# Kernel tuning notes

Measured on AMD Instinct MI355X. Metric: run time of the kernel, lower is better.

Reference implementation:

```python
import jax, jax.numpy as jnp
import numpy as np

B, T, C, H = 2, 2048, 1024, 16
D = C // H  # head_dim = 64


def setup_inputs() -> dict:
    key = jax.random.key(0)
    ks = jax.random.split(key, 5)
    x = jax.random.normal(ks[0], (B, T, C), dtype=jnp.float32)
    # fused QKV projection: Linear(C, 3C)
    W_qkv = jax.random.normal(ks[1], (C, 3 * C), dtype=jnp.float32) / np.sqrt(C)
    b_qkv = jax.random.normal(ks[2], (3 * C,), dtype=jnp.float32) * 0.02
    # output projection: Linear(C, C)
    W_proj = jax.random.normal(ks[3], (C, C), dtype=jnp.float32) / np.sqrt(C)
    b_proj = jax.random.normal(ks[4], (C,), dtype=jnp.float32) * 0.02
    return {"x": x, "W_qkv": W_qkv, "b_qkv": b_qkv, "W_proj": W_proj, "b_proj": b_proj}


def reference(x, W_qkv, b_qkv, W_proj, b_proj):
    # fused QKV projection
    qkv = jnp.einsum("btc,cd->btd", x, W_qkv) + b_qkv  # [B,T,3C]
    q, k, v = jnp.split(qkv, 3, axis=-1)
    # [B,T,C] -> [B,H,T,D]
    def to_heads(t):
        return t.reshape(B, T, H, D).transpose(0, 2, 1, 3)
    q, k, v = to_heads(q), to_heads(k), to_heads(v)
    # causal scaled dot-product attention (SDPA default scale = 1/sqrt(head_dim))
    scale = 1.0 / np.sqrt(D).astype(np.float32)
    scores = jnp.einsum("bhqd,bhkd->bhqk", q, k) * scale  # [B,H,T,T]
    causal = jnp.tril(jnp.ones((T, T), dtype=bool))
    scores = jnp.where(causal, scores, jnp.finfo(scores.dtype).min)
    attn = jax.nn.softmax(scores, axis=-1)
    out = jnp.einsum("bhqk,bhkd->bhqd", attn, v)  # [B,H,T,D]
    out = out.transpose(0, 2, 1, 3).reshape(B, T, C)
    # output projection
    return jnp.einsum("btc,cd->btd", out, W_proj) + b_proj
```

## Files before the change

kernel.cpp:

```cpp
#include <hip/hip_runtime.h>
#include <hip/hip_bf16.h>

typedef __attribute__((ext_vector_type(8))) __bf16 bf16x8;
typedef __attribute__((ext_vector_type(8))) short short8;
typedef __attribute__((ext_vector_type(4))) float f32x4;
typedef __attribute__((ext_vector_type(4))) short sh4;

typedef __attribute__((address_space(1))) void GVoid;
typedef __attribute__((address_space(3))) void LVoid;

#define NEGBIG (-1e30f)
#define SCL 0.18033688011112042f

constexpr int TT = 2048, CC = 1024, HH = 16, DD = 64, C3 = 3072;

__device__ __forceinline__ unsigned short f2bf(float f) {
  unsigned int i = __float_as_uint(f);
  return (unsigned short)((i + 0x7FFFu + ((i >> 16) & 1u)) >> 16);
}
__device__ __forceinline__ unsigned short f2bf_tr(float f) {
  return (unsigned short)(__float_as_uint(f) >> 16);
}
__device__ __forceinline__ void async16(const void* g, void* l) {
  __builtin_amdgcn_global_load_lds((GVoid*)g, (LVoid*)l, 16, 0, 0);
}

__global__ __launch_bounds__(256) void cvt_bf16(
    const float* __restrict__ in, unsigned short* __restrict__ out, int n8)
{
  const int i = blockIdx.x * 256 + threadIdx.x;
  if (i >= n8) return;
  const float* p = in + (size_t)i * 8;
  f32x4 a = *(const f32x4*)p, b = *(const f32x4*)(p + 4);
  sh4 r0, r1;
  ((unsigned short*)&r0)[0] = f2bf(a[0]); ((unsigned short*)&r0)[1] = f2bf(a[1]);
  ((unsigned short*)&r0)[2] = f2bf(a[2]); ((unsigned short*)&r0)[3] = f2bf(a[3]);
  ((unsigned short*)&r1)[0] = f2bf(b[0]); ((unsigned short*)&r1)[1] = f2bf(b[1]);
  ((unsigned short*)&r1)[2] = f2bf(b[2]); ((unsigned short*)&r1)[3] = f2bf(b[3]);
  *(sh4*)(out + (size_t)i * 8) = r0;
  *(sh4*)(out + (size_t)i * 8 + 4) = r1;
}

__global__ __launch_bounds__(256) void transpose_cvt(
    const float* __restrict__ in, unsigned short* __restrict__ out, int R, int Cd)
{
  __shared__ __align__(16) unsigned short tile[64 * 72];
  const int r0 = blockIdx.y * 64, c0 = blockIdx.x * 64;
  const int tid = threadIdx.x;
#pragma unroll
  for (int r = 0; r < 2; ++r) {
    const int elem = r * 2048 + tid * 8;
    const int ii = elem >> 6, jj = elem & 63;
    const float* p = in + (size_t)(r0 + ii) * Cd + c0 + jj;
    f32x4 a = *(const f32x4*)p, b = *(const f32x4*)(p + 4);
    short8 v;
    ((unsigned short*)&v)[0] = f2bf(a[0]); ((unsigned short*)&v)[1] = f2bf(a[1]);
    ((unsigned short*)&v)[2] = f2bf(a[2]); ((unsigned short*)&v)[3] = f2bf(a[3]);
    ((unsigned short*)&v)[4] = f2bf(b[0]); ((unsigned short*)&v)[5] = f2bf(b[1]);
    ((unsigned short*)&v)[6] = f2bf(b[2]); ((unsigned short*)&v)[7] = f2bf(b[3]);
    *(short8*)&tile[ii * 72 + jj] = v;
  }
  __syncthreads();
#pragma unroll
  for (int r = 0; r < 2; ++r) {
    const int elem = r * 2048 + tid * 8;
    const int jj = elem >> 6, ii0 = elem & 63;
    short8 v;
#pragma unroll
    for (int e = 0; e < 8; ++e) ((unsigned short*)&v)[e] = tile[(ii0 + e) * 72 + jj];
    *(short8*)&out[(size_t)(c0 + jj) * R + r0 + ii0] = v;
  }
}

template <int MODE>
__global__ __launch_bounds__(256) void gemm_bt(
    const unsigned short* __restrict__ A,
    const unsigned short* __restrict__ Bt,
    const float* __restrict__ bias,
    void* __restrict__ Cp, unsigned short* __restrict__ Vt,
    int M, int N, int K, int lda)
{
  __shared__ __align__(16) unsigned short sA[128 * 32];
  __shared__ __align__(16) unsigned short sB[128 * 32];
  const int tid = threadIdx.x;
  const int w = tid >> 6, l = tid & 63, ln = l & 15, quad = l >> 4;
  const int wm = w >> 1, wn = w & 1;
  const int m0 = blockIdx.y * 128, n0 = blockIdx.x * 128;
  f32x4 acc[4][4] = {};

  for (int k0 = 0; k0 < K; k0 += 32) {
    __syncthreads();
#pragma unroll
    for (int r = 0; r < 2; ++r) {
      const int elem = r * 2048 + tid * 8;
      const int ar = elem >> 5, ac = elem & 31;
      async16(A  + (size_t)(m0 + ar) * lda + k0 + ac, sA + r * 2048 + w * 512);
      async16(Bt + (size_t)(n0 + ar) * K   + k0 + ac, sB + r * 2048 + w * 512);
    }
    __syncthreads();

    bf16x8 af[4], bfr[4];
#pragma unroll
    for (int i = 0; i < 4; i++)
      af[i] = *(const bf16x8*)&sA[(wm * 64 + i * 16 + ln) * 32 + quad * 8];
#pragma unroll
    for (int j = 0; j < 4; j++)
      bfr[j] = *(const bf16x8*)&sB[(wn * 64 + j * 16 + ln) * 32 + quad * 8];
#pragma unroll
    for (int i = 0; i < 4; i++)
#pragma unroll
      for (int j = 0; j < 4; j++)
        acc[i][j] = __builtin_amdgcn_mfma_f32_16x16x32_bf16(af[i], bfr[j], acc[i][j], 0, 0, 0);
  }

  float bj[4];
#pragma unroll
  for (int j = 0; j < 4; j++) bj[j] = bias[n0 + wn * 64 + j * 16 + ln];

#pragma unroll
  for (int i = 0; i < 4; i++)
#pragma unroll
    for (int g = 0; g < 4; ++g) {
      const int gm = m0 + wm * 64 + i * 16 + quad * 4 + g;
#pragma unroll
      for (int j = 0; j < 4; j++) {
        const int gn = n0 + wn * 64 + j * 16 + ln;
        float v = acc[i][j][g] + bj[j];
        if (MODE == 0) {
          if (gn < 2048) {
            if (gn < 1024) v *= SCL;
            ((unsigned short*)Cp)[(size_t)gm * 2048 + gn] = f2bf(v);
          } else {
            const int hh = (gn >> 6) & 15, dd = gn & 63;
            const int bb = gm >> 11, t = gm & 2047;
            Vt[((size_t)((bb * HH + hh) * DD + dd)) * TT + t] = f2bf(v);
          }
        } else {
          ((float*)Cp)[(size_t)gm * N + gn] = v;
        }
      }
    }
}

__global__ __launch_bounds__(512) void attn128(
    unsigned short* __restrict__ QK, const unsigned short* __restrict__ Vt)
{
  __shared__ __align__(16) unsigned short kt[2][64 * 72];
  __shared__ __align__(16) unsigned short vt[2][80 * 72];
  __shared__ __align__(16) unsigned short pt[8][16 * 72];
  const int pair = blockIdx.x, bh = blockIdx.y;
  const int b = bh >> 4, h = bh & 15;
  const int tid = threadIdx.x, w = tid >> 6, l = tid & 63, ln = l & 15, quad = l >> 4;
  unsigned short*       Qp = QK + (size_t)b * TT * 2048 + h * DD;
  const unsigned short* Kp = QK + (size_t)b * TT * 2048 + CC + h * DD;
  const unsigned short* Vh = Vt + (size_t)bh * DD * TT;
  const int si = tid >> 3, so = (tid & 7) * 8;

  for (int idx = tid; idx < 16 * 72; idx += 512) {
    const unsigned short v = (idx < 72) ? (unsigned short)0x3F80 : (unsigned short)0;
    vt[0][64 * 72 + idx] = v;
    vt[1][64 * 72 + idx] = v;
  }

  for (int ph = 0; ph < 2; ++ph) {
    const int qt = ph ? 15 - pair : pair;
    const int qrow = qt * 128 + w * 16 + ln;
    bf16x8 qf0 = *(const bf16x8*)&Qp[(size_t)qrow * 2048 + quad * 8];
    bf16x8 qf1 = *(const bf16x8*)&Qp[(size_t)qrow * 2048 + 32 + quad * 8];

    f32x4 oacc[4] = {};
    f32x4 lacc = {};
    const int qg = qt * 128 + w * 16 + quad * 4;
    const int wfirst = qt * 128 + w * 16, wlast = wfirst + 15;
    const int kbmax = 2 * qt + 1;

    *(short8*)&kt[0][si * 72 + so] = *(const short8*)&Kp[(size_t)si * 2048 + so];
    *(short8*)&vt[0][si * 72 + so] = *(const short8*)&Vh[(size_t)si * TT + so];
    __syncthreads();

    for (int kb = 0; kb <= kbmax; ++kb) {
      const int cur = kb & 1;
      short8 pk, pv;
      if (kb < kbmax) {
        pk = *(const short8*)&Kp[(size_t)((kb + 1) * 64 + si) * 2048 + so];
        pv = *(const short8*)&Vh[(size_t)si * TT + (kb + 1) * 64 + so];
      }
      if (kb * 64 <= wlast) {
        f32x4 sacc[4] = {};
#pragma unroll
        for (int n = 0; n < 4; n++) {
          bf16x8 bk0 = *(const bf16x8*)&kt[cur][(n * 16 + ln) * 72 + quad * 8];
          bf16x8 bk1 = *(const bf16x8*)&kt[cur][(n * 16 + ln) * 72 + 32 + quad * 8];
          sacc[n] = __builtin_amdgcn_mfma_f32_16x16x32_bf16(qf0, bk0, sacc[n], 0, 0, 0);
          sacc[n] = __builtin_amdgcn_mfma_f32_16x16x32_bf16(qf1, bk1, sacc[n], 0, 0, 0);
        }
        if (kb * 64 + 63 > wfirst) {
#pragma unroll
          for (int n = 0; n < 4; n++) {
            const int keyg = kb * 64 + n * 16 + ln;
#pragma unroll
            for (int g = 0; g < 4; ++g)
              if (keyg > qg + g) sacc[n][g] = NEGBIG;
          }
        }
#pragma unroll
        for (int n = 0; n < 4; n++)
#pragma unroll
          for (int g = 0; g < 4; ++g)
            pt[w][(quad * 4 + g) * 72 + n * 16 + ln] = f2bf_tr(exp2f(sacc[n][g]));
        __builtin_amdgcn_wave_barrier();
        bf16x8 pf0 = *(const bf16x8*)&pt[w][ln * 72 + quad * 8];
        bf16x8 pf1 = *(const bf16x8*)&pt[w][ln * 72 + 32 + quad * 8];
#pragma unroll
        for (int n = 0; n < 4; n++) {
          bf16x8 bv0 = *(const bf16x8*)&vt[cur][(n * 16 + ln) * 72 + quad * 8];
          bf16x8 bv1 = *(const bf16x8*)&vt[cur][(n * 16 + ln) * 72 + 32 + quad * 8];
          oacc[n] = __builtin_amdgcn_mfma_f32_16x16x32_bf16(pf0, bv0, oacc[n], 0, 0, 0);
          oacc[n] = __builtin_amdgcn_mfma_f32_16x16x32_bf16(pf1, bv1, oacc[n], 0, 0, 0);
        }
        bf16x8 bl0 = *(const bf16x8*)&vt[cur][(64 + ln) * 72 + quad * 8];
        bf16x8 bl1 = *(const bf16x8*)&vt[cur][(64 + ln) * 72 + 32 + quad * 8];
        lacc = __builtin_amdgcn_mfma_f32_16x16x32_bf16(pf0, bl0, lacc, 0, 0, 0);
        lacc = __builtin_amdgcn_mfma_f32_16x16x32_bf16(pf1, bl1, lacc, 0, 0, 0);
      }
      if (kb < kbmax) {
        *(short8*)&kt[1 - cur][si * 72 + so] = pk;
        *(short8*)&vt[1 - cur][si * 72 + so] = pv;
      }
      __syncthreads();
    }
#pragma unroll
    for (int g = 0; g < 4; ++g) {
      const float lv = __shfl(lacc[g], l & 48);
      const float inv = 1.0f / lv;
      const int t = qg + g;
#pragma unroll
      for (int n = 0; n < 4; n++)
        Qp[(size_t)t * 2048 + n * 16 + ln] = f2bf(oacc[n][g] * inv);
    }
  }
}

extern "C" void kernel_launch(void* const* d_in, const int* in_sizes, int n_in,
                              void* d_out, int out_size, void* d_ws, size_t ws_size,
                              hipStream_t stream)
{
  (void)in_sizes; (void)n_in; (void)out_size; (void)ws_size;
  const float* x     = (const float*)d_in[0];
  const float* Wqkv  = (const float*)d_in[1];
  const float* bqkv  = (const float*)d_in[2];
  const float* Wproj = (const float*)d_in[3];
  const float* bproj = (const float*)d_in[4];

  unsigned short* QK     = (unsigned short*)d_ws;
  unsigned short* WqkvT  = QK + (size_t)4096 * 2048;
  unsigned short* WprojT = WqkvT;
  unsigned short* Vt = (unsigned short*)d_out;
  unsigned short* xb = Vt + (size_t)32 * 64 * 2048;

  cvt_bf16<<<dim3(4096 * 1024 / 8 / 256), 256, 0, stream>>>(x, xb, 4096 * 1024 / 8);
  transpose_cvt<<<dim3(C3 / 64, CC / 64), 256, 0, stream>>>(Wqkv, WqkvT, CC, C3);
  gemm_bt<0><<<dim3(C3 / 128, 4096 / 128), 256, 0, stream>>>(
      xb, WqkvT, bqkv, QK, Vt, 4096, C3, CC, CC);
  transpose_cvt<<<dim3(CC / 64, CC / 64), 256, 0, stream>>>(Wproj, WprojT, CC, CC);
  attn128<<<dim3(8, 2 * HH), 512, 0, stream>>>(QK, Vt);
  gemm_bt<1><<<dim3(CC / 128, 4096 / 128), 256, 0, stream>>>(
      QK, WprojT, bproj, d_out, nullptr, 4096, CC, CC, 2048);
}
```

Measured before the change: 208.7 us.

## Split attention into 64-row query tiles with heaviest-first block order

The attention kernel moves from 512-thread blocks that each process two paired 128-row query tiles to 256-thread blocks that each process one 64-row tile. Tiles are launched in reverse order so the longest causal tiles start first, and the grid grows from 256 to 1024 blocks. The aim is more blocks to spread across CUs and finer load balancing than the old pairing gave. In exchange, each K/V block staged in shared memory is reused by fewer query rows, so total K/V traffic roughly doubles.

```diff
diff --git a/kernel.cpp b/kernel.cpp
--- a/kernel.cpp
+++ b/kernel.cpp
@@ -142,102 +142,111 @@
     }
 }
 
-__global__ __launch_bounds__(512) void attn128(
+__global__ __launch_bounds__(256) void attn64(
     unsigned short* __restrict__ QK, const unsigned short* __restrict__ Vt)
 {
   __shared__ __align__(16) unsigned short kt[2][64 * 72];
   __shared__ __align__(16) unsigned short vt[2][80 * 72];
-  __shared__ __align__(16) unsigned short pt[8][16 * 72];
-  const int pair = blockIdx.x, bh = blockIdx.y;
+  __shared__ __align__(16) unsigned short pt[4][16 * 72];
+  const int tile = 31 - blockIdx.x;
+  const int bh = blockIdx.y;
   const int b = bh >> 4, h = bh & 15;
   const int tid = threadIdx.x, w = tid >> 6, l = tid & 63, ln = l & 15, quad = l >> 4;
   unsigned short*       Qp = QK + (size_t)b * TT * 2048 + h * DD;
   const unsigned short* Kp = QK + (size_t)b * TT * 2048 + CC + h * DD;
   const unsigned short* Vh = Vt + (size_t)bh * DD * TT;
-  const int si = tid >> 3, so = (tid & 7) * 8;
-
-  for (int idx = tid; idx < 16 * 72; idx += 512) {
+  const int si0 = tid >> 3, so = (tid & 7) * 8;
+
+  for (int idx = tid; idx < 16 * 72; idx += 256) {
     const unsigned short v = (idx < 72) ? (unsigned short)0x3F80 : (unsigned short)0;
     vt[0][64 * 72 + idx] = v;
     vt[1][64 * 72 + idx] = v;
   }
 
-  for (int ph = 0; ph < 2; ++ph) {
-    const int qt = ph ? 15 - pair : pair;
-    const int qrow = qt * 128 + w * 16 + ln;
-    bf16x8 qf0 = *(const bf16x8*)&Qp[(size_t)qrow * 2048 + quad * 8];
-    bf16x8 qf1 = *(const bf16x8*)&Qp[(size_t)qrow * 2048 + 32 + quad * 8];
-
-    f32x4 oacc[4] = {};
-    f32x4 lacc = {};
-    const int qg = qt * 128 + w * 16 + quad * 4;
-    const int wfirst = qt * 128 + w * 16, wlast = wfirst + 15;
-    const int kbmax = 2 * qt + 1;
-
+  const int qrow = tile * 64 + w * 16 + ln;
+  bf16x8 qf0 = *(const bf16x8*)&Qp[(size_t)qrow * 2048 + quad * 8];
+  bf16x8 qf1 = *(const bf16x8*)&Qp[(size_t)qrow * 2048 + 32 + quad * 8];
+
+  f32x4 oacc[4] = {};
+  f32x4 lacc = {};
+  const int qg = tile * 64 + w * 16 + quad * 4;
+  const int kbmax = tile;
+
+#pragma unroll
+  for (int r = 0; r < 2; ++r) {
+    const int si = si0 + 32 * r;
     *(short8*)&kt[0][si * 72 + so] = *(const short8*)&Kp[(size_t)si * 2048 + so];
     *(short8*)&vt[0][si * 72 + so] = *(const short8*)&Vh[(size_t)si * TT + so];
+  }
+  __syncthreads();
+
+  for (int kb = 0; kb <= kbmax; ++kb) {
+    const int cur = kb & 1;
+    short8 pk[2], pv[2];
+    if (kb < kbmax) {
+#pragma unroll
+      for (int r = 0; r < 2; ++r) {
+        const int si = si0 + 32 * r;
+        pk[r] = *(const short8*)&Kp[(size_t)((kb + 1) * 64 + si) * 2048 + so];
+        pv[r] = *(const short8*)&Vh[(size_t)si * TT + (kb + 1) * 64 + so];
+      }
+    }
+    {
+      f32x4 sacc[4] = {};
+#pragma unroll
+      for (int n = 0; n < 4; n++) {
+        bf16x8 bk0 = *(const bf16x8*)&kt[cur][(n * 16 + ln) * 72 + quad * 8];
+        bf16x8 bk1 = *(const bf16x8*)&kt[cur][(n * 16 + ln) * 72 + 32 + quad * 8];
+        sacc[n] = __builtin_amdgcn_mfma_f32_16x16x32_bf16(qf0, bk0, sacc[n], 0, 0, 0);
+        sacc[n] = __builtin_amdgcn_mfma_f32_16x16x32_bf16(qf1, bk1, sacc[n], 0, 0, 0);
+      }
+      if (kb == kbmax) {
+#pragma unroll
+        for (int n = 0; n < 4; n++) {
+          const int keyg = kb * 64 + n * 16 + ln;
+#pragma unroll
+          for (int g = 0; g < 4; ++g)
+            if (keyg > qg + g) sacc[n][g] = NEGBIG;
+        }
+      }
+#pragma unroll
+      for (int n = 0; n < 4; n++)
+#pragma unroll
+        for (int g = 0; g < 4; ++g)
+          pt[w][(quad * 4 + g) * 72 + n * 16 + ln] = f2bf_tr(exp2f(sacc[n][g]));
+      __builtin_amdgcn_wave_barrier();
+      bf16x8 pf0 = *(const bf16x8*)&pt[w][ln * 72 + quad * 8];
+      bf16x8 pf1 = *(const bf16x8*)&pt[w][ln * 72 + 32 + quad * 8];
+#pragma unroll
+      for (int n = 0; n < 4; n++) {
+        bf16x8 bv0 = *(const bf16x8*)&vt[cur][(n * 16 + ln) * 72 + quad * 8];
+        bf16x8 bv1 = *(const bf16x8*)&vt[cur][(n * 16 + ln) * 72 + 32 + quad * 8];
+        oacc[n] = __builtin_amdgcn_mfma_f32_16x16x32_bf16(pf0, bv0, oacc[n], 0, 0, 0);
+        oacc[n] = __builtin_amdgcn_mfma_f32_16x16x32_bf16(pf1, bv1, oacc[n], 0, 0, 0);
+      }
+      bf16x8 bl0 = *(const bf16x8*)&vt[cur][(64 + ln) * 72 + quad * 8];
+      bf16x8 bl1 = *(const bf16x8*)&vt[cur][(64 + ln) * 72 + 32 + quad * 8];
+      lacc = __builtin_amdgcn_mfma_f32_16x16x32_bf16(pf0, bl0, lacc, 0, 0, 0);
+      lacc = __builtin_amdgcn_mfma_f32_16x16x32_bf16(pf1, bl1, lacc, 0, 0, 0);
+    }
+    if (kb < kbmax) {
+#pragma unroll
+      for (int r = 0; r < 2; ++r) {
+        const int si = si0 + 32 * r;
+        *(short8*)&kt[1 - cur][si * 72 + so] = pk[r];
+        *(short8*)&vt[1 - cur][si * 72 + so] = pv[r];
+      }
+    }
     __syncthreads();
-
-    for (int kb = 0; kb <= kbmax; ++kb) {
-      const int cur = kb & 1;
-      short8 pk, pv;
-      if (kb < kbmax) {
-        pk = *(const short8*)&Kp[(size_t)((kb + 1) * 64 + si) * 2048 + so];
-        pv = *(const short8*)&Vh[(size_t)si * TT + (kb + 1) * 64 + so];
-      }
-      if (kb * 64 <= wlast) {
-        f32x4 sacc[4] = {};
-#pragma unroll
-        for (int n = 0; n < 4; n++) {
-          bf16x8 bk0 = *(const bf16x8*)&kt[cur][(n * 16 + ln) * 72 + quad * 8];
-          bf16x8 bk1 = *(const bf16x8*)&kt[cur][(n * 16 + ln) * 72 + 32 + quad * 8];
-          sacc[n] = __builtin_amdgcn_mfma_f32_16x16x32_bf16(qf0, bk0, sacc[n], 0, 0, 0);
-          sacc[n] = __builtin_amdgcn_mfma_f32_16x16x32_bf16(qf1, bk1, sacc[n], 0, 0, 0);
-        }
-        if (kb * 64 + 63 > wfirst) {
-#pragma unroll
-          for (int n = 0; n < 4; n++) {
-            const int keyg = kb * 64 + n * 16 + ln;
-#pragma unroll
-            for (int g = 0; g < 4; ++g)
-              if (keyg > qg + g) sacc[n][g] = NEGBIG;
-          }
-        }
-#pragma unroll
-        for (int n = 0; n < 4; n++)
-#pragma unroll
-          for (int g = 0; g < 4; ++g)
-            pt[w][(quad * 4 + g) * 72 + n * 16 + ln] = f2bf_tr(exp2f(sacc[n][g]));
-        __builtin_amdgcn_wave_barrier();
-        bf16x8 pf0 = *(const bf16x8*)&pt[w][ln * 72 + quad * 8];
-        bf16x8 pf1 = *(const bf16x8*)&pt[w][ln * 72 + 32 + quad * 8];
-#pragma unroll
-        for (int n = 0; n < 4; n++) {
-          bf16x8 bv0 = *(const bf16x8*)&vt[cur][(n * 16 + ln) * 72 + quad * 8];
-          bf16x8 bv1 = *(const bf16x8*)&vt[cur][(n * 16 + ln) * 72 + 32 + quad * 8];
-          oacc[n] = __builtin_amdgcn_mfma_f32_16x16x32_bf16(pf0, bv0, oacc[n], 0, 0, 0);
-          oacc[n] = __builtin_amdgcn_mfma_f32_16x16x32_bf16(pf1, bv1, oacc[n], 0, 0, 0);
-        }
-        bf16x8 bl0 = *(const bf16x8*)&vt[cur][(64 + ln) * 72 + quad * 8];
-        bf16x8 bl1 = *(const bf16x8*)&vt[cur][(64 + ln) * 72 + 32 + quad * 8];
-        lacc = __builtin_amdgcn_mfma_f32_16x16x32_bf16(pf0, bl0, lacc, 0, 0, 0);
-        lacc = __builtin_amdgcn_mfma_f32_16x16x32_bf16(pf1, bl1, lacc, 0, 0, 0);
-      }
-      if (kb < kbmax) {
-        *(short8*)&kt[1 - cur][si * 72 + so] = pk;
-        *(short8*)&vt[1 - cur][si * 72 + so] = pv;
-      }
-      __syncthreads();
-    }
-#pragma unroll
-    for (int g = 0; g < 4; ++g) {
-      const float lv = __shfl(lacc[g], l & 48);
-      const float inv = 1.0f / lv;
-      const int t = qg + g;
-#pragma unroll
-      for (int n = 0; n < 4; n++)
-        Qp[(size_t)t * 2048 + n * 16 + ln] = f2bf(oacc[n][g] * inv);
-    }
+  }
+#pragma unroll
+  for (int g = 0; g < 4; ++g) {
+    const float lv = __shfl(lacc[g], l & 48);
+    const float inv = 1.0f / lv;
+    const int t = qg + g;
+#pragma unroll
+    for (int n = 0; n < 4; n++)
+      Qp[(size_t)t * 2048 + n * 16 + ln] = f2bf(oacc[n][g] * inv);
   }
 }
 
@@ -263,7 +272,7 @@
   gemm_bt<0><<<dim3(C3 / 128, 4096 / 128), 256, 0, stream>>>(
       xb, WqkvT, bqkv, QK, Vt, 4096, C3, CC, CC);
   transpose_cvt<<<dim3(CC / 64, CC / 64), 256, 0, stream>>>(Wproj, WprojT, CC, CC);
-  attn128<<<dim3(8, 2 * HH), 512, 0, stream>>>(QK, Vt);
+  attn64<<<dim3(32, 2 * HH), 256, 0, stream>>>(QK, Vt);
   gemm_bt<1><<<dim3(CC / 128, 4096 / 128), 256, 0, stream>>>(
       QK, WprojT, bproj, d_out, nullptr, 4096, CC, CC, 2048);
 }
```

Measured after the change: 243.6 us. +16.7%, slower.

## Software-pipeline PV MFMA one block behind QK and compute row sums in VALU

Applied to the files above, without the earlier changes.

Restructures the attention inner loop so the P·V matmul for the previous key block runs while the current block's QK scores and exp are computed. V tiles move to a triple buffer to support the one-step lag. The ones-row MFMA trick for the softmax denominator is replaced by summing the fp32 exponentials in registers and reducing across lanes with xor shuffles. This shortens the per-iteration dependency chain and removes two MFMAs per block, at the cost of more LDS and register pressure. The row sum now uses the fp32 values rather than the truncated bf16 ones used in P·V, which slightly changes numerics.

```diff
diff --git a/kernel.cpp b/kernel.cpp
--- a/kernel.cpp
+++ b/kernel.cpp
@@ -146,7 +146,7 @@
     unsigned short* __restrict__ QK, const unsigned short* __restrict__ Vt)
 {
   __shared__ __align__(16) unsigned short kt[2][64 * 72];
-  __shared__ __align__(16) unsigned short vt[2][80 * 72];
+  __shared__ __align__(16) unsigned short vt[3][64 * 72];
   __shared__ __align__(16) unsigned short pt[8][16 * 72];
   const int pair = blockIdx.x, bh = blockIdx.y;
   const int b = bh >> 4, h = bh & 15;
@@ -156,12 +156,6 @@
   const unsigned short* Vh = Vt + (size_t)bh * DD * TT;
   const int si = tid >> 3, so = (tid & 7) * 8;
 
-  for (int idx = tid; idx < 16 * 72; idx += 512) {
-    const unsigned short v = (idx < 72) ? (unsigned short)0x3F80 : (unsigned short)0;
-    vt[0][64 * 72 + idx] = v;
-    vt[1][64 * 72 + idx] = v;
-  }
-
   for (int ph = 0; ph < 2; ++ph) {
     const int qt = ph ? 15 - pair : pair;
     const int qrow = qt * 128 + w * 16 + ln;
@@ -170,30 +164,46 @@
 
     f32x4 oacc[4] = {};
     f32x4 lacc = {};
+    bf16x8 pf0 = {}, pf1 = {};
     const int qg = qt * 128 + w * 16 + quad * 4;
     const int wfirst = qt * 128 + w * 16, wlast = wfirst + 15;
     const int kbmax = 2 * qt + 1;
-
+    int vm1 = 2, v0 = 0, vp1 = 1;
+
+    __syncthreads();
     *(short8*)&kt[0][si * 72 + so] = *(const short8*)&Kp[(size_t)si * 2048 + so];
     *(short8*)&vt[0][si * 72 + so] = *(const short8*)&Vh[(size_t)si * TT + so];
     __syncthreads();
 
     for (int kb = 0; kb <= kbmax; ++kb) {
-      const int cur = kb & 1;
+      const int ck = kb & 1;
       short8 pk, pv;
       if (kb < kbmax) {
         pk = *(const short8*)&Kp[(size_t)((kb + 1) * 64 + si) * 2048 + so];
         pv = *(const short8*)&Vh[(size_t)si * TT + (kb + 1) * 64 + so];
       }
-      if (kb * 64 <= wlast) {
-        f32x4 sacc[4] = {};
+      const bool qk_act = (kb * 64 <= wlast);
+      f32x4 sacc[4] = {};
+      if (qk_act) {
 #pragma unroll
         for (int n = 0; n < 4; n++) {
-          bf16x8 bk0 = *(const bf16x8*)&kt[cur][(n * 16 + ln) * 72 + quad * 8];
-          bf16x8 bk1 = *(const bf16x8*)&kt[cur][(n * 16 + ln) * 72 + 32 + quad * 8];
+          bf16x8 bk0 = *(const bf16x8*)&kt[ck][(n * 16 + ln) * 72 + quad * 8];
+          bf16x8 bk1 = *(const bf16x8*)&kt[ck][(n * 16 + ln) * 72 + 32 + quad * 8];
           sacc[n] = __builtin_amdgcn_mfma_f32_16x16x32_bf16(qf0, bk0, sacc[n], 0, 0, 0);
           sacc[n] = __builtin_amdgcn_mfma_f32_16x16x32_bf16(qf1, bk1, sacc[n], 0, 0, 0);
         }
+      }
+      if (kb > 0 && (kb - 1) * 64 <= wlast) {
+        const unsigned short* vp = vt[vm1];
+#pragma unroll
+        for (int n = 0; n < 4; n++) {
+          bf16x8 bv0 = *(const bf16x8*)&vp[(n * 16 + ln) * 72 + quad * 8];
+          bf16x8 bv1 = *(const bf16x8*)&vp[(n * 16 + ln) * 72 + 32 + quad * 8];
+          oacc[n] = __builtin_amdgcn_mfma_f32_16x16x32_bf16(pf0, bv0, oacc[n], 0, 0, 0);
+          oacc[n] = __builtin_amdgcn_mfma_f32_16x16x32_bf16(pf1, bv1, oacc[n], 0, 0, 0);
+        }
+      }
+      if (qk_act) {
         if (kb * 64 + 63 > wfirst) {
 #pragma unroll
           for (int n = 0; n < 4; n++) {
@@ -203,36 +213,48 @@
               if (keyg > qg + g) sacc[n][g] = NEGBIG;
           }
         }
+        float pe[4][4];
 #pragma unroll
         for (int n = 0; n < 4; n++)
 #pragma unroll
+          for (int g = 0; g < 4; ++g) pe[n][g] = exp2f(sacc[n][g]);
+#pragma unroll
+        for (int g = 0; g < 4; ++g)
+          lacc[g] += (pe[0][g] + pe[1][g]) + (pe[2][g] + pe[3][g]);
+#pragma unroll
+        for (int n = 0; n < 4; n++)
+#pragma unroll
           for (int g = 0; g < 4; ++g)
-            pt[w][(quad * 4 + g) * 72 + n * 16 + ln] = f2bf_tr(exp2f(sacc[n][g]));
+            pt[w][(quad * 4 + g) * 72 + n * 16 + ln] = f2bf_tr(pe[n][g]);
         __builtin_amdgcn_wave_barrier();
-        bf16x8 pf0 = *(const bf16x8*)&pt[w][ln * 72 + quad * 8];
-        bf16x8 pf1 = *(const bf16x8*)&pt[w][ln * 72 + 32 + quad * 8];
-#pragma unroll
-        for (int n = 0; n < 4; n++) {
-          bf16x8 bv0 = *(const bf16x8*)&vt[cur][(n * 16 + ln) * 72 + quad * 8];
-          bf16x8 bv1 = *(const bf16x8*)&vt[cur][(n * 16 + ln) * 72 + 32 + quad * 8];
-          oacc[n] = __builtin_amdgcn_mfma_f32_16x16x32_bf16(pf0, bv0, oacc[n], 0, 0, 0);
-          oacc[n] = __builtin_amdgcn_mfma_f32_16x16x32_bf16(pf1, bv1, oacc[n], 0, 0, 0);
-        }
-        bf16x8 bl0 = *(const bf16x8*)&vt[cur][(64 + ln) * 72 + quad * 8];
-        bf16x8 bl1 = *(const bf16x8*)&vt[cur][(64 + ln) * 72 + 32 + quad * 8];
-        lacc = __builtin_amdgcn_mfma_f32_16x16x32_bf16(pf0, bl0, lacc, 0, 0, 0);
-        lacc = __builtin_amdgcn_mfma_f32_16x16x32_bf16(pf1, bl1, lacc, 0, 0, 0);
+        pf0 = *(const bf16x8*)&pt[w][ln * 72 + quad * 8];
+        pf1 = *(const bf16x8*)&pt[w][ln * 72 + 32 + quad * 8];
       }
       if (kb < kbmax) {
-        *(short8*)&kt[1 - cur][si * 72 + so] = pk;
-        *(short8*)&vt[1 - cur][si * 72 + so] = pv;
+        *(short8*)&kt[1 - ck][si * 72 + so] = pk;
+        *(short8*)&vt[vp1][si * 72 + so] = pv;
       }
       __syncthreads();
+      const int t_ = vm1; vm1 = v0; v0 = vp1; vp1 = t_;
+    }
+    if (kbmax * 64 <= wlast) {
+      const unsigned short* vp = vt[vm1];
+#pragma unroll
+      for (int n = 0; n < 4; n++) {
+        bf16x8 bv0 = *(const bf16x8*)&vp[(n * 16 + ln) * 72 + quad * 8];
+        bf16x8 bv1 = *(const bf16x8*)&vp[(n * 16 + ln) * 72 + 32 + quad * 8];
+        oacc[n] = __builtin_amdgcn_mfma_f32_16x16x32_bf16(pf0, bv0, oacc[n], 0, 0, 0);
+        oacc[n] = __builtin_amdgcn_mfma_f32_16x16x32_bf16(pf1, bv1, oacc[n], 0, 0, 0);
+      }
     }
 #pragma unroll
     for (int g = 0; g < 4; ++g) {
-      const float lv = __shfl(lacc[g], l & 48);
-      const float inv = 1.0f / lv;
+      float s = lacc[g];
+      s += __shfl_xor(s, 1);
+      s += __shfl_xor(s, 2);
+      s += __shfl_xor(s, 4);
+      s += __shfl_xor(s, 8);
+      const float inv = 1.0f / s;
       const int t = qg + g;
 #pragma unroll
       for (int n = 0; n < 4; n++)
```

New measurement: 204.9 us. Within noise of the previous version (-1.8%).
